# Kernel tuning notes

Measured on AMD Instinct MI355X. Metric: run time of the kernel, lower is better.

The kernel has to match this reference:

```python
import jax, jax.numpy as jnp
import numpy as np

ALPHA = 0.2  # LeakyReLU negative slope
NEG_BIG = -9e15


def setup_inputs() -> dict:
    key = jax.random.key(0)
    k1, k2, k3, k4 = jax.random.split(key, 4)
    B, N, Fin, Fout = 16, 1024, 256, 256
    h = jax.random.normal(k1, (B, N, Fin), dtype=jnp.float32)
    adj = jax.random.randint(k2, (B, N, N), 0, 2, dtype=jnp.int32)
    # xavier_uniform with gain=1.414
    def xavier(k, shape, gain=1.414):
        fan_in, fan_out = shape[0], shape[1]
        bound = gain * np.sqrt(6.0 / (fan_in + fan_out))
        return jax.random.uniform(k, shape, jnp.float32, -bound, bound)
    W = xavier(k3, (Fin, Fout))
    a = xavier(k4, (2 * Fout, 1))
    return {"h": h, "adj": adj, "W": W, "a": a}


def reference(h, adj, W, a):
    # h: [B,N,Fin], adj: [B,N,N], W: [Fin,Fout], a: [2*Fout,1]
    Fout = W.shape[1]
    Wh = jnp.einsum('bnf,fo->bno', h, W)                      # [B,N,Fout]
    a1, a2 = a[:Fout, 0], a[Fout:, 0]                          # [Fout], [Fout]
    # e_ij = leakyrelu(Wh_i . a1 + Wh_j . a2) -- outer sum, no O(N^2*F) tensor
    f1 = Wh @ a1                                               # [B,N]
    f2 = Wh @ a2                                               # [B,N]
    e = jax.nn.leaky_relu(f1[:, :, None] + f2[:, None, :], negative_slope=ALPHA)
    attention = jnp.where(adj > 0, e, jnp.float32(NEG_BIG))    # [B,N,N]
    attention = jax.nn.softmax(attention, axis=2)
    h_prime = jnp.einsum('bij,bjo->bio', attention, Wh)        # [B,N,Fout]
    return jax.nn.elu(h_prime)
```

## Files before the change

kernel.cpp:

```cpp
#include <hip/hip_runtime.h>
#include <hip/hip_bf16.h>

#define Bsz 16
#define Nn  1024
#define Ff  256
#define ALPHA 0.2f
#define NEG_BIG -9.0e15f

typedef __attribute__((ext_vector_type(8))) short short8;
typedef __attribute__((ext_vector_type(4))) float f32x4;
typedef __attribute__((ext_vector_type(4))) unsigned short ushort4_t;

__device__ __forceinline__ unsigned short f2bf(float x) {
    union { __hip_bfloat16 b; unsigned short u; } cv;
    cv.b = __float2bfloat16(x);
    return cv.u;
}

__global__ __launch_bounds__(256) void gat_prep(
    const float* __restrict__ W, const float* __restrict__ a,
    float* __restrict__ w1, float* __restrict__ w2)
{
    const int t = threadIdx.x, w = t >> 6, ln = t & 63;
    __shared__ float a1s[Ff], a2s[Ff];
    a1s[t] = a[t];
    a2s[t] = a[Ff + t];
    __syncthreads();
    const int f = blockIdx.x * 4 + w;
    float s1 = 0.f, s2 = 0.f;
    #pragma unroll
    for (int c = 0; c < 4; c++) {
        const int o = ln + 64 * c;
        const float wv = W[(size_t)f * Ff + o];
        s1 += wv * a1s[o];
        s2 += wv * a2s[o];
    }
    #pragma unroll
    for (int off = 1; off < 64; off <<= 1) {
        s1 += __shfl_xor(s1, off, 64);
        s2 += __shfl_xor(s2, off, 64);
    }
    if (ln == 0) { w1[f] = s1; w2[f] = s2; }
}

__global__ __launch_bounds__(256) void pack_f(
    const float* __restrict__ h, const float* __restrict__ W,
    const float* __restrict__ w1, const float* __restrict__ w2,
    unsigned short* __restrict__ hK, unsigned short* __restrict__ WK,
    float* __restrict__ f1, float* __restrict__ f2)
{
    __shared__ __align__(16) float tile[32][260];
    const int id = blockIdx.x, t = threadIdx.x, w = t >> 6, ln = t & 63;
    const bool isH = (id < 512);
    const float* src;
    unsigned short* dst;
    int grow0 = 0;
    if (isH) {
        const int b = id >> 5, kt = id & 31;
        grow0 = b * Nn + kt * 32;
        src = h + (size_t)grow0 * Ff;
        dst = hK + ((size_t)(b * 32 + kt)) * 8192;
    } else {
        const int ft = id - 512;
        src = W + (size_t)ft * 32 * Ff;
        dst = WK + (size_t)ft * 8192;
    }
    #pragma unroll
    for (int rr = 0; rr < 8; rr++) {
        const int row = rr * 4 + w;
        const int col = ln * 4;
        *(float4*)&tile[row][col] = *(const float4*)&src[row * Ff + col];
    }
    __syncthreads();

    unsigned* d32 = (unsigned*)dst;
    #pragma unroll
    for (int k = 0; k < 16; k++) {
        const int fidx = k * 256 + t;
        const int o = fidx >> 4, q = fidx & 15;
        const unsigned lo = f2bf(tile[2 * q][o]);
        const unsigned hi = f2bf(tile[2 * q + 1][o]);
        d32[fidx] = lo | (hi << 16);
    }

    if (isH) {
        float w1r[4], w2r[4];
        #pragma unroll
        for (int c = 0; c < 4; c++) {
            w1r[c] = w1[ln + 64 * c];
            w2r[c] = w2[ln + 64 * c];
        }
        #pragma unroll
        for (int rr = 0; rr < 8; rr++) {
            const int row = rr * 4 + w;
            float s1 = 0.f, s2 = 0.f;
            #pragma unroll
            for (int c = 0; c < 4; c++) {
                const float hv = tile[row][ln + 64 * c];
                s1 += hv * w1r[c];
                s2 += hv * w2r[c];
            }
            #pragma unroll
            for (int off = 1; off < 64; off <<= 1) {
                s1 += __shfl_xor(s1, off, 64);
                s2 += __shfl_xor(s2, off, 64);
            }
            if (ln == 0) { f1[grow0 + row] = s1; f2[grow0 + row] = s2; }
        }
    }
}

#define TI 32
__global__ __launch_bounds__(1024, 8) void gat_attn(
    const int* __restrict__ adj,
    const float* __restrict__ f1, const float* __restrict__ f2,
    const unsigned short* __restrict__ hK, const unsigned short* __restrict__ WK,
    float* __restrict__ out)
{
    __shared__ __align__(16) unsigned short pbf[TI * 1024];
    const int t = threadIdx.x, w = t >> 6, ln = t & 63;
    const int m = ln & 15, quad = ln >> 4;
    const int bid = blockIdx.x;
    const int b  = 2 * (bid & 7) + ((bid >> 3) & 1);
    const int i0 = (bid >> 4) * TI;

    float4 f2r[4];
    #pragma unroll
    for (int c = 0; c < 4; c++)
        f2r[c] = *(const float4*)&f2[b * Nn + 256 * c + 4 * ln];

    const int r0 = 2 * w, r1 = r0 + 1;
    const int grb = b * Nn + i0 + r0;
    const int* aptr = adj + (size_t)grb * Nn;
    int4 av0[4], av1[4];
    #pragma unroll
    for (int c = 0; c < 4; c++) {
        av0[c] = *(const int4*)&aptr[c * 256 + 4 * ln];
        av1[c] = *(const int4*)&aptr[Nn + c * 256 + 4 * ln];
    }
    const float fi0 = f1[grb], fi1 = f1[grb + 1];
    float e0[16], e1[16];
    float mx0 = -INFINITY, mx1 = -INFINITY;
    #pragma unroll
    for (int c = 0; c < 4; c++) {
        const float4 fv = f2r[c];
        float x, y;
        x = fi0 + fv.x; x = fmaxf(x, ALPHA * x); x = av0[c].x > 0 ? x : NEG_BIG; e0[4*c+0] = x;
        y = fi0 + fv.y; y = fmaxf(y, ALPHA * y); y = av0[c].y > 0 ? y : NEG_BIG; e0[4*c+1] = y;
        mx0 = fmaxf(fmaxf(x, y), mx0);
        x = fi0 + fv.z; x = fmaxf(x, ALPHA * x); x = av0[c].z > 0 ? x : NEG_BIG; e0[4*c+2] = x;
        y = fi0 + fv.w; y = fmaxf(y, ALPHA * y); y = av0[c].w > 0 ? y : NEG_BIG; e0[4*c+3] = y;
        mx0 = fmaxf(fmaxf(x, y), mx0);
        x = fi1 + fv.x; x = fmaxf(x, ALPHA * x); x = av1[c].x > 0 ? x : NEG_BIG; e1[4*c+0] = x;
        y = fi1 + fv.y; y = fmaxf(y, ALPHA * y); y = av1[c].y > 0 ? y : NEG_BIG; e1[4*c+1] = y;
        mx1 = fmaxf(fmaxf(x, y), mx1);
        x = fi1 + fv.z; x = fmaxf(x, ALPHA * x); x = av1[c].z > 0 ? x : NEG_BIG; e1[4*c+2] = x;
        y = fi1 + fv.w; y = fmaxf(y, ALPHA * y); y = av1[c].w > 0 ? y : NEG_BIG; e1[4*c+3] = y;
        mx1 = fmaxf(fmaxf(x, y), mx1);
    }
    #pragma unroll
    for (int off = 1; off < 64; off <<= 1) {
        mx0 = fmaxf(mx0, __shfl_xor(mx0, off, 64));
        mx1 = fmaxf(mx1, __shfl_xor(mx1, off, 64));
    }
    float s0 = 0.f, s1 = 0.f;
    #pragma unroll
    for (int c = 0; c < 16; c++) {
        e0[c] = __expf(e0[c] - mx0); s0 += e0[c];
        e1[c] = __expf(e1[c] - mx1); s1 += e1[c];
    }
    #pragma unroll
    for (int off = 1; off < 64; off <<= 1) {
        s0 += __shfl_xor(s0, off, 64);
        s1 += __shfl_xor(s1, off, 64);
    }
    const float ri0 = 1.f / s0, ri1 = 1.f / s1;
    #pragma unroll
    for (int c = 0; c < 4; c++) {
        const int j = 256 * c + 4 * ln;
        ushort4_t v0 = { f2bf(e0[4*c] * ri0), f2bf(e0[4*c+1] * ri0),
                         f2bf(e0[4*c+2] * ri0), f2bf(e0[4*c+3] * ri0) };
        ushort4_t v1 = { f2bf(e1[4*c] * ri1), f2bf(e1[4*c+1] * ri1),
                         f2bf(e1[4*c+2] * ri1), f2bf(e1[4*c+3] * ri1) };
        *(ushort4_t*)&pbf[r0 * 1024 + (j ^ ((r0 & 7) << 3))] = v0;
        *(ushort4_t*)&pbf[r1 * 1024 + (j ^ ((r1 & 7) << 3))] = v1;
    }
    __syncthreads();

    const int n0 = w * 16;
    const unsigned short* hKb = hK + (size_t)b * 32 * 8192;
    const int arow0 = m * 1024, arow1 = (16 + m) * 1024;
    const int asw = (m & 7) << 3;
    #define AF0(kt) (*(const short8*)&pbf[arow0 + ((((kt) * 32) + quad * 8) ^ asw)])
    #define AF1(kt) (*(const short8*)&pbf[arow1 + ((((kt) * 32) + quad * 8) ^ asw)])
    #define BF(kt)  (*(const short8*)&hKb[(size_t)(kt) * 8192 + (n0 + m) * 32 + quad * 8])

    f32x4 acc0 = {0.f,0.f,0.f,0.f}, acc1 = acc0;
    short8 a0c = AF0(0), a1c = AF1(0);
    short8 bc = BF(0), bn = BF(1);
    #pragma unroll
    for (int kt = 0; kt < 32; kt++) {
        short8 bnn = bc, a0n = a0c, a1n = a1c;
        if (kt + 2 < 32) bnn = BF(kt + 2);
        if (kt + 1 < 32) { a0n = AF0(kt + 1); a1n = AF1(kt + 1); }
        acc0 = __builtin_amdgcn_mfma_f32_16x16x32_bf16(a0c, bc, acc0, 0, 0, 0);
        acc1 = __builtin_amdgcn_mfma_f32_16x16x32_bf16(a1c, bc, acc1, 0, 0, 0);
        a0c = a0n; a1c = a1n; bc = bn; bn = bnn;
    }

    __syncthreads();
    #pragma unroll
    for (int reg = 0; reg < 4; reg++) {
        pbf[(quad * 4 + reg) * 264 + n0 + m]      = f2bf(acc0[reg]);
        pbf[(16 + quad * 4 + reg) * 264 + n0 + m] = f2bf(acc1[reg]);
    }
    __syncthreads();

    #define GA0(kt) (*(const short8*)&pbf[m * 264 + (kt) * 32 + quad * 8])
    #define GA1(kt) (*(const short8*)&pbf[(16 + m) * 264 + (kt) * 32 + quad * 8])
    #define WB(kt)  (*(const short8*)&WK[(size_t)(kt) * 8192 + (n0 + m) * 32 + quad * 8])

    f32x4 c0 = {0.f,0.f,0.f,0.f}, c1 = c0;
    short8 ga0 = GA0(0), ga1 = GA1(0), wb = WB(0);
    #pragma unroll
    for (int kt = 0; kt < 8; kt++) {
        short8 ga0n = ga0, ga1n = ga1, wbn = wb;
        if (kt + 1 < 8) { ga0n = GA0(kt + 1); ga1n = GA1(kt + 1); wbn = WB(kt + 1); }
        c0 = __builtin_amdgcn_mfma_f32_16x16x32_bf16(ga0, wb, c0, 0, 0, 0);
        c1 = __builtin_amdgcn_mfma_f32_16x16x32_bf16(ga1, wb, c1, 0, 0, 0);
        ga0 = ga0n; ga1 = ga1n; wb = wbn;
    }
    const size_t ob = (size_t)(b * Nn) + i0;
    #pragma unroll
    for (int reg = 0; reg < 4; reg++) {
        float v;
        v = c0[reg]; v = v > 0.f ? v : (__expf(v) - 1.f);
        out[(ob + quad * 4 + reg) * Ff + n0 + m] = v;
        v = c1[reg]; v = v > 0.f ? v : (__expf(v) - 1.f);
        out[(ob + 16 + quad * 4 + reg) * Ff + n0 + m] = v;
    }
}

extern "C" void kernel_launch(void* const* d_in, const int* in_sizes, int n_in,
                              void* d_out, int out_size, void* d_ws, size_t ws_size,
                              hipStream_t stream)
{
    const void* h   = d_in[0];
    const void* adj = d_in[1];
    const void* W   = d_in[2];
    const void* a   = d_in[3];
    for (int i = 0; i < n_in; i++) {
        if      (in_sizes[i] == Bsz * Nn * Ff) h   = d_in[i];
        else if (in_sizes[i] == Bsz * Nn * Nn) adj = d_in[i];
        else if (in_sizes[i] == Ff * Ff)       W   = d_in[i];
        else if (in_sizes[i] == 2 * Ff)        a   = d_in[i];
    }
    float* out = (float*)d_out;

    char*  wsb = (char*)d_ws;
    float* w1  = (float*)wsb;
    float* w2  = w1 + Ff;
    float* f1  = (float*)(wsb + 4096);
    float* f2  = f1 + Bsz * Nn;
    unsigned short* hK = (unsigned short*)(wsb + 4096 + 2 * 65536);
    unsigned short* WK = hK + (size_t)Bsz * 32 * 8192;

    gat_prep<<<64, 256, 0, stream>>>((const float*)W, (const float*)a, w1, w2);
    pack_f<<<520, 256, 0, stream>>>((const float*)h, (const float*)W, w1, w2, hK, WK, f1, f2);
    gat_attn<<<Bsz * (Nn / TI), 1024, 0, stream>>>((const int*)adj, f1, f2, hK, WK, out);
}
```

Before: 136.7 us.

## Use analytic row max bound and deferred softmax normalization in GAT attention

Replaces the per-row softmax max reduction with an upper bound computed from the global max of f2 (LeakyReLU is monotonic), removing one cross-lane max reduction per row and the temporary e arrays. Exponentials use exp2 with pre-scaled inputs, and masked entries become zero instead of going through NEG_BIG. Normalization by the row sum is deferred until after the attention matmul, where the row sums are read from shared memory and applied with a fast reciprocal. The risk is numerical: the bound may sit well above the true row max, so rows whose valid entries are all small could underflow, and unnormalized values are quantized to bf16.

```diff
diff --git a/kernel.cpp b/kernel.cpp
--- a/kernel.cpp
+++ b/kernel.cpp
@@ -6,6 +6,7 @@
 #define Ff  256
 #define ALPHA 0.2f
 #define NEG_BIG -9.0e15f
+#define LOG2E 1.44269504f
 
 typedef __attribute__((ext_vector_type(8))) short short8;
 typedef __attribute__((ext_vector_type(4))) float f32x4;
@@ -15,6 +16,22 @@
     union { __hip_bfloat16 b; unsigned short u; } cv;
     cv.b = __float2bfloat16(x);
     return cv.u;
+}
+
+__device__ __forceinline__ float exp2_fast(float x) {
+#if __has_builtin(__builtin_amdgcn_exp2f)
+    return __builtin_amdgcn_exp2f(x);
+#else
+    return exp2f(x);
+#endif
+}
+
+__device__ __forceinline__ float rcp_fast(float x) {
+#if __has_builtin(__builtin_amdgcn_rcpf)
+    return __builtin_amdgcn_rcpf(x);
+#else
+    return 1.f / x;
+#endif
 }
 
 __global__ __launch_bounds__(256) void gat_prep(
@@ -118,17 +135,13 @@
     float* __restrict__ out)
 {
     __shared__ __align__(16) unsigned short pbf[TI * 1024];
+    __shared__ __align__(16) float ss[TI];
     const int t = threadIdx.x, w = t >> 6, ln = t & 63;
     const int m = ln & 15, quad = ln >> 4;
     const int bid = blockIdx.x;
     const int b  = 2 * (bid & 7) + ((bid >> 3) & 1);
     const int i0 = (bid >> 4) * TI;
 
-    float4 f2r[4];
-    #pragma unroll
-    for (int c = 0; c < 4; c++)
-        f2r[c] = *(const float4*)&f2[b * Nn + 256 * c + 4 * ln];
-
     const int r0 = 2 * w, r1 = r0 + 1;
     const int grb = b * Nn + i0 + r0;
     const int* aptr = adj + (size_t)grb * Nn;
@@ -138,53 +151,60 @@
         av0[c] = *(const int4*)&aptr[c * 256 + 4 * ln];
         av1[c] = *(const int4*)&aptr[Nn + c * 256 + 4 * ln];
     }
+
+    float4 f2r[4];
+    #pragma unroll
+    for (int c = 0; c < 4; c++)
+        f2r[c] = *(const float4*)&f2[b * Nn + 256 * c + 4 * ln];
+
+    float mx2 = fmaxf(fmaxf(f2r[0].x, f2r[0].y), fmaxf(f2r[0].z, f2r[0].w));
+    #pragma unroll
+    for (int c = 1; c < 4; c++)
+        mx2 = fmaxf(mx2, fmaxf(fmaxf(f2r[c].x, f2r[c].y), fmaxf(f2r[c].z, f2r[c].w)));
+    #pragma unroll
+    for (int off = 1; off < 64; off <<= 1)
+        mx2 = fmaxf(mx2, __shfl_xor(mx2, off, 64));
+
+    #pragma unroll
+    for (int c = 0; c < 4; c++) {
+        f2r[c].x *= LOG2E; f2r[c].y *= LOG2E;
+        f2r[c].z *= LOG2E; f2r[c].w *= LOG2E;
+    }
+
     const float fi0 = f1[grb], fi1 = f1[grb + 1];
-    float e0[16], e1[16];
-    float mx0 = -INFINITY, mx1 = -INFINITY;
+    float q0 = fi0 + mx2; q0 = fmaxf(q0, ALPHA * q0);
+    float q1 = fi1 + mx2; q1 = fmaxf(q1, ALPHA * q1);
+    const float mx0L = q0 * LOG2E, mx1L = q1 * LOG2E;
+    const float fi0L = fi0 * LOG2E, fi1L = fi1 * LOG2E;
+    const int sw0 = (r0 & 7) << 3, sw1 = (r1 & 7) << 3;
+
+    float s0 = 0.f, s1 = 0.f;
     #pragma unroll
     for (int c = 0; c < 4; c++) {
         const float4 fv = f2r[c];
-        float x, y;
-        x = fi0 + fv.x; x = fmaxf(x, ALPHA * x); x = av0[c].x > 0 ? x : NEG_BIG; e0[4*c+0] = x;
-        y = fi0 + fv.y; y = fmaxf(y, ALPHA * y); y = av0[c].y > 0 ? y : NEG_BIG; e0[4*c+1] = y;
-        mx0 = fmaxf(fmaxf(x, y), mx0);
-        x = fi0 + fv.z; x = fmaxf(x, ALPHA * x); x = av0[c].z > 0 ? x : NEG_BIG; e0[4*c+2] = x;
-        y = fi0 + fv.w; y = fmaxf(y, ALPHA * y); y = av0[c].w > 0 ? y : NEG_BIG; e0[4*c+3] = y;
-        mx0 = fmaxf(fmaxf(x, y), mx0);
-        x = fi1 + fv.x; x = fmaxf(x, ALPHA * x); x = av1[c].x > 0 ? x : NEG_BIG; e1[4*c+0] = x;
-        y = fi1 + fv.y; y = fmaxf(y, ALPHA * y); y = av1[c].y > 0 ? y : NEG_BIG; e1[4*c+1] = y;
-        mx1 = fmaxf(fmaxf(x, y), mx1);
-        x = fi1 + fv.z; x = fmaxf(x, ALPHA * x); x = av1[c].z > 0 ? x : NEG_BIG; e1[4*c+2] = x;
-        y = fi1 + fv.w; y = fmaxf(y, ALPHA * y); y = av1[c].w > 0 ? y : NEG_BIG; e1[4*c+3] = y;
-        mx1 = fmaxf(fmaxf(x, y), mx1);
-    }
-    #pragma unroll
-    for (int off = 1; off < 64; off <<= 1) {
-        mx0 = fmaxf(mx0, __shfl_xor(mx0, off, 64));
-        mx1 = fmaxf(mx1, __shfl_xor(mx1, off, 64));
-    }
-    float s0 = 0.f, s1 = 0.f;
-    #pragma unroll
-    for (int c = 0; c < 16; c++) {
-        e0[c] = __expf(e0[c] - mx0); s0 += e0[c];
-        e1[c] = __expf(e1[c] - mx1); s1 += e1[c];
+        float x, p00, p01, p02, p03, p10, p11, p12, p13;
+        x = fi0L + fv.x; x = fmaxf(x, ALPHA * x); p00 = exp2_fast(x - mx0L); p00 = av0[c].x > 0 ? p00 : 0.f;
+        x = fi0L + fv.y; x = fmaxf(x, ALPHA * x); p01 = exp2_fast(x - mx0L); p01 = av0[c].y > 0 ? p01 : 0.f;
+        x = fi0L + fv.z; x = fmaxf(x, ALPHA * x); p02 = exp2_fast(x - mx0L); p02 = av0[c].z > 0 ? p02 : 0.f;
+        x = fi0L + fv.w; x = fmaxf(x, ALPHA * x); p03 = exp2_fast(x - mx0L); p03 = av0[c].w > 0 ? p03 : 0.f;
+        x = fi1L + fv.x; x = fmaxf(x, ALPHA * x); p10 = exp2_fast(x - mx1L); p10 = av1[c].x > 0 ? p10 : 0.f;
+        x = fi1L + fv.y; x = fmaxf(x, ALPHA * x); p11 = exp2_fast(x - mx1L); p11 = av1[c].y > 0 ? p11 : 0.f;
+        x = fi1L + fv.z; x = fmaxf(x, ALPHA * x); p12 = exp2_fast(x - mx1L); p12 = av1[c].z > 0 ? p12 : 0.f;
+        x = fi1L + fv.w; x = fmaxf(x, ALPHA * x); p13 = exp2_fast(x - mx1L); p13 = av1[c].w > 0 ? p13 : 0.f;
+        s0 += (p00 + p01) + (p02 + p03);
+        s1 += (p10 + p11) + (p12 + p13);
+        const int j = 256 * c + 4 * ln;
+        ushort4_t v0 = { f2bf(p00), f2bf(p01), f2bf(p02), f2bf(p03) };
+        ushort4_t v1 = { f2bf(p10), f2bf(p11), f2bf(p12), f2bf(p13) };
+        *(ushort4_t*)&pbf[r0 * 1024 + (j ^ sw0)] = v0;
+        *(ushort4_t*)&pbf[r1 * 1024 + (j ^ sw1)] = v1;
     }
     #pragma unroll
     for (int off = 1; off < 64; off <<= 1) {
         s0 += __shfl_xor(s0, off, 64);
         s1 += __shfl_xor(s1, off, 64);
     }
-    const float ri0 = 1.f / s0, ri1 = 1.f / s1;
-    #pragma unroll
-    for (int c = 0; c < 4; c++) {
-        const int j = 256 * c + 4 * ln;
-        ushort4_t v0 = { f2bf(e0[4*c] * ri0), f2bf(e0[4*c+1] * ri0),
-                         f2bf(e0[4*c+2] * ri0), f2bf(e0[4*c+3] * ri0) };
-        ushort4_t v1 = { f2bf(e1[4*c] * ri1), f2bf(e1[4*c+1] * ri1),
-                         f2bf(e1[4*c+2] * ri1), f2bf(e1[4*c+3] * ri1) };
-        *(ushort4_t*)&pbf[r0 * 1024 + (j ^ ((r0 & 7) << 3))] = v0;
-        *(ushort4_t*)&pbf[r1 * 1024 + (j ^ ((r1 & 7) << 3))] = v1;
-    }
+    if (ln == 0) { ss[r0] = s0; ss[r1] = s1; }
     __syncthreads();
 
     const int n0 = w * 16;
@@ -208,11 +228,16 @@
         a0c = a0n; a1c = a1n; bc = bn; bn = bnn;
     }
 
+    const f32x4 sv0 = *(const f32x4*)&ss[quad * 4];
+    const f32x4 sv1 = *(const f32x4*)&ss[16 + quad * 4];
+
     __syncthreads();
     #pragma unroll
     for (int reg = 0; reg < 4; reg++) {
-        pbf[(quad * 4 + reg) * 264 + n0 + m]      = f2bf(acc0[reg]);
-        pbf[(16 + quad * 4 + reg) * 264 + n0 + m] = f2bf(acc1[reg]);
+        const float i0s = rcp_fast(fmaxf(sv0[reg], 1e-30f));
+        const float i1s = rcp_fast(fmaxf(sv1[reg], 1e-30f));
+        pbf[(quad * 4 + reg) * 264 + n0 + m]      = f2bf(acc0[reg] * i0s);
+        pbf[(16 + quad * 4 + reg) * 264 + n0 + m] = f2bf(acc1[reg] * i1s);
     }
     __syncthreads();
 
```

Measured after the change: 143.7 us. 1.05x slower.
